# Kernel tuning notes

Hardware: AMD Instinct MI355X
Metric: run time of the kernel (lower is better)

Reference implementation:

```python
import jax, jax.numpy as jnp
import numpy as np

X_DIM = 512
Y_DIM = 512
HID = 300
N = 2048


def setup_inputs() -> dict:
    key = jax.random.key(0)
    ks = jax.random.split(key, 8)
    scale = 0.05
    return {
        "pos_local": jax.random.normal(ks[0], (N, X_DIM), jnp.float32),
        "pos_global": jax.random.normal(ks[1], (N, Y_DIM), jnp.float32),
        "neg_local": jax.random.normal(ks[2], (N, X_DIM), jnp.float32),
        "neg_global": jax.random.normal(ks[3], (N, Y_DIM), jnp.float32),
        "W1": jax.random.normal(ks[4], (X_DIM + Y_DIM, HID), jnp.float32) * scale,
        "b1": jnp.zeros((HID,), jnp.float32),
        "W2": jax.random.normal(ks[5], (HID, 1), jnp.float32) * scale,
        "b2": jnp.zeros((1,), jnp.float32),
        "batch_size": 256,
    }


def reference(pos_local, pos_global, neg_local, neg_global, W1, b1, W2, b2, batch_size):
    # Split first-layer weight into local/global halves so we never materialize
    # the concatenated pair tensor: F(cat(l, g)) uses l @ W1l + g @ W1g.
    W1l, W1g = W1[:X_DIM], W1[X_DIM:]
    w2, bias2 = W2[:, 0], b2[0]

    # Positive branch: plain batched MLP, chunking does not change the math.
    h0 = jax.nn.relu(pos_local @ W1l + pos_global @ W1g + b1)  # [N, HID]
    t0 = jax.nn.softplus(h0 @ w2 + bias2).mean()

    # Negative branch: per chunk of size B, pair (local_j, global_i),
    # score[i, j] = F(local_j, global_i); logsumexp over j, mean over i.
    nc = neg_local.shape[0] // batch_size
    nl = neg_local.reshape(nc, batch_size, X_DIM)
    ng = neg_global.reshape(nc, batch_size, Y_DIM)

    def chunk_term(carry, lg):
        l, g = lg                                   # [B, x], [B, y]
        lp = l @ W1l                                # [B, HID]
        gp = g @ W1g                                # [B, HID]
        h = jax.nn.relu(gp[:, None, :] + lp[None, :, :] + b1)  # [B, B, HID]
        s = jax.nn.softplus(h @ w2 + bias2)         # [B, B]
        val = jax.scipy.special.logsumexp(s, axis=1).mean()
        return carry + val, None

    total, _ = jax.lax.scan(chunk_term, jnp.float32(0.0), (nl, ng))
    t1 = total / nc

    lower_bound = t0 - t1
    return -lower_bound
```

## Files before the change

kernel.cpp:

```cpp
#include <hip/hip_runtime.h>
#include <math.h>

#define NR   2048
#define XD   512
#define HID  300
#define BS   256
#define NPAD 320
#define KTOT 1024
#define GSTR 304
#define HSTR 304
#define KP   320
#define NNEG 256

typedef __attribute__((ext_vector_type(8))) short bf16x8;
typedef __attribute__((ext_vector_type(4))) float f32x4;

__device__ __forceinline__ float softplus_f(float x) {
    return fmaxf(x, 0.f) + log1pf(__expf(-fabsf(x)));
}
__device__ __forceinline__ unsigned short f2bf(float f) {
    unsigned int u = __float_as_uint(f);
    u += 0x7FFFu + ((u >> 16) & 1u);
    return (unsigned short)(u >> 16);
}
__device__ __forceinline__ float bf2f(unsigned short h) {
    return __uint_as_float((unsigned int)h << 16);
}
__device__ __forceinline__ void unpk(unsigned int u, float& lo, float& hi) {
    lo = __uint_as_float(u << 16);
    hi = __uint_as_float(u & 0xFFFF0000u);
}

__global__ __launch_bounds__(256) void convert(
    const float* __restrict__ pl, const float* __restrict__ pg,
    const float* __restrict__ nl, const float* __restrict__ ng,
    const float* __restrict__ W1,
    unsigned short* __restrict__ Aneg, unsigned short* __restrict__ Apos,
    unsigned short* __restrict__ Wt, unsigned int* __restrict__ counter)
{
    const int b = blockIdx.x, tid = threadIdx.x;
    if (b == 0 && tid == 0) *counter = 0u;
    if (b < 4096) {
        const int m = (b < 2048) ? b : b - 2048;
        const float* lo = (b < 2048) ? nl : pl;
        const float* hi = (b < 2048) ? ng : pg;
        unsigned short* dst = (b < 2048) ? Aneg : Apos;
        const int kq = tid * 4;
        const float4 v = (kq < XD) ? *(const float4*)(lo + m * XD + kq)
                                   : *(const float4*)(hi + m * XD + kq - XD);
        ushort4 o;
        o.x = f2bf(v.x); o.y = f2bf(v.y); o.z = f2bf(v.z); o.w = f2bf(v.w);
        *(ushort4*)(dst + m * KTOT + kq) = o;
    } else {
        __shared__ unsigned short ts[16][72];
        const int t = b - 4096;
        const int nt = t % 20, kt = t / 20;
        const int n = nt * 16 + (tid & 15);
        const int kl = tid >> 4;
        #pragma unroll
        for (int j = 0; j < 4; ++j) {
            const int k = kt * 64 + kl * 4 + j;
            ts[tid & 15][kl * 4 + j] = f2bf((n < HID) ? W1[k * HID + n] : 0.f);
        }
        __syncthreads();
        const int nw = tid >> 4, kw = (tid & 15) * 4;
        ushort4 o;
        o.x = ts[nw][kw]; o.y = ts[nw][kw + 1]; o.z = ts[nw][kw + 2]; o.w = ts[nw][kw + 3];
        *(ushort4*)(Wt + (nt * 16 + nw) * KTOT + kt * 64 + kw) = o;
    }
}

__global__ __launch_bounds__(64) void mfma_gemm(
    const unsigned short* __restrict__ Aneg, const unsigned short* __restrict__ Apos,
    const unsigned short* __restrict__ Wt, const float* __restrict__ b1,
    unsigned short* __restrict__ LP4h, unsigned short* __restrict__ GPBh,
    float* __restrict__ P0a, float* __restrict__ P0b)
{
    const int bid = blockIdx.x;
    const int job = bid / 160, t = bid % 160;
    const int m0 = (t & 31) * 64, n0 = (t >> 5) * 64;
    const int lane = threadIdx.x;
    const int r = lane & 15, g = lane >> 4;

    const unsigned short* A = (job >= 2) ? Apos : Aneg;
    const int kbeg = (job & 1) ? XD : 0;

    const unsigned short* ap[4];
    const unsigned short* bp[4];
    #pragma unroll
    for (int mi = 0; mi < 4; ++mi)
        ap[mi] = A + (m0 + 16 * mi + r) * KTOT + kbeg + 8 * g;
    #pragma unroll
    for (int ni = 0; ni < 4; ++ni)
        bp[ni] = Wt + (n0 + 16 * ni + r) * KTOT + kbeg + 8 * g;

    f32x4 acc[4][4] = {};

    #pragma unroll 4
    for (int k = 0; k < XD; k += 32) {
        bf16x8 a[4], w[4];
        #pragma unroll
        for (int mi = 0; mi < 4; ++mi) a[mi] = *(const bf16x8*)(ap[mi] + k);
        #pragma unroll
        for (int ni = 0; ni < 4; ++ni) w[ni] = *(const bf16x8*)(bp[ni] + k);
        #pragma unroll
        for (int mi = 0; mi < 4; ++mi)
            #pragma unroll
            for (int ni = 0; ni < 4; ++ni)
                acc[mi][ni] = __builtin_amdgcn_mfma_f32_16x16x32_bf16(
                    a[mi], w[ni], acc[mi][ni], 0, 0, 0);
    }

    #pragma unroll
    for (int mi = 0; mi < 4; ++mi) {
        #pragma unroll
        for (int ni = 0; ni < 4; ++ni) {
            const int n = n0 + ni * 16 + r;
            const int mb = m0 + mi * 16 + 4 * g;
            const f32x4 v = acc[mi][ni];
            if (job == 0) {
                unsigned short* base = LP4h + ((size_t)(n >> 3) * NR + mb) * 8 + (n & 7);
                base[0]  = f2bf(v[0]); base[8]  = f2bf(v[1]);
                base[16] = f2bf(v[2]); base[24] = f2bf(v[3]);
            } else if (n < HID) {
                if (job == 1) {
                    const float bias = b1[n];
                    #pragma unroll
                    for (int j = 0; j < 4; ++j)
                        GPBh[(size_t)(mb + j) * HSTR + n] = f2bf(v[j] + bias);
                } else {
                    float* out = (job == 2) ? P0a : P0b;
                    #pragma unroll
                    for (int j = 0; j < 4; ++j)
                        out[(size_t)(mb + j) * GSTR + n] = v[j];
                }
            }
        }
    }
}

__global__ __launch_bounds__(512, 2) void negpos(
    const unsigned short* __restrict__ LP4h, const unsigned short* __restrict__ GPBh,
    const float* __restrict__ P0a, const float* __restrict__ P0b,
    const float* __restrict__ b1, const float* __restrict__ W2,
    const float* __restrict__ b2,
    float* __restrict__ negE, float* __restrict__ posP,
    unsigned int* __restrict__ counter, float* __restrict__ out)
{
    __shared__ __align__(16) float w2s[KP];
    __shared__ __align__(16) float gbs[8][KP];
    __shared__ __align__(16) float pacc[8][BS][8];
    __shared__ float sC[8];
    __shared__ float red[4][8];
    __shared__ float redp[8];
    __shared__ int sh_last;
    const int tid = threadIdx.x, bid = blockIdx.x;
    const int kh = tid >> 6, lh = tid & 63;
    const float b2v = b2[0];
    const int chunk = bid >> 5, g0 = (bid & 31) * 8;
    const size_t cb = (size_t)chunk * BS;

    const unsigned short* gpb = GPBh + (cb + g0) * HSTR;
    if (tid < KP) {
        const bool v = tid < HID;
        w2s[tid] = v ? 0.5f * W2[tid] : 0.f;
        #pragma unroll
        for (int g = 0; g < 8; ++g)
            gbs[g][tid] = v ? bf2f(gpb[g * HSTR + tid]) : 0.f;
    }
    __syncthreads();

    {
        float c = 0.f;
        #pragma unroll
        for (int h = 0; h < 2; ++h) {
            const int k4 = lh + 64 * h;
            if (k4 < 80) {
                const float4 g4 = *(const float4*)&gbs[kh][k4 * 4];
                const float4 w4 = *(const float4*)&w2s[k4 * 4];
                c += g4.x * w4.x + g4.y * w4.y + g4.z * w4.z + g4.w * w4.w;
            }
        }
        #pragma unroll
        for (int o = 32; o > 0; o >>= 1) c += __shfl_xor(c, o);
        if (lh == 0) sC[kh] = c;
    }

    float acc[8][4];
    float q[4] = {0.f, 0.f, 0.f, 0.f};
    #pragma unroll
    for (int gt = 0; gt < 8; ++gt)
        #pragma unroll
        for (int j = 0; j < 4; ++j) acc[gt][j] = 0.f;

    #pragma unroll
    for (int i = 0; i < 5; ++i) {
        const int k8 = 5 * kh + i;
        uint4 u0 = *(const uint4*)(LP4h + ((size_t)k8 * NR + cb + lh)       * 8);
        uint4 u1 = *(const uint4*)(LP4h + ((size_t)k8 * NR + cb + lh + 64)  * 8);
        uint4 u2 = *(const uint4*)(LP4h + ((size_t)k8 * NR + cb + lh + 128) * 8);
        uint4 u3 = *(const uint4*)(LP4h + ((size_t)k8 * NR + cb + lh + 192) * 8);
        const float4 wa = *(const float4*)&w2s[k8 * 8];
        const float4 wb = *(const float4*)&w2s[k8 * 8 + 4];
        float fv[4][8];
        unpk(u0.x, fv[0][0], fv[0][1]); unpk(u0.y, fv[0][2], fv[0][3]);
        unpk(u0.z, fv[0][4], fv[0][5]); unpk(u0.w, fv[0][6], fv[0][7]);
        unpk(u1.x, fv[1][0], fv[1][1]); unpk(u1.y, fv[1][2], fv[1][3]);
        unpk(u1.z, fv[1][4], fv[1][5]); unpk(u1.w, fv[1][6], fv[1][7]);
        unpk(u2.x, fv[2][0], fv[2][1]); unpk(u2.y, fv[2][2], fv[2][3]);
        unpk(u2.z, fv[2][4], fv[2][5]); unpk(u2.w, fv[2][6], fv[2][7]);
        unpk(u3.x, fv[3][0], fv[3][1]); unpk(u3.y, fv[3][2], fv[3][3]);
        unpk(u3.z, fv[3][4], fv[3][5]); unpk(u3.w, fv[3][6], fv[3][7]);
        #pragma unroll
        for (int j = 0; j < 4; ++j) {
            q[j] = fmaf(wa.x, fv[j][0], q[j]); q[j] = fmaf(wa.y, fv[j][1], q[j]);
            q[j] = fmaf(wa.z, fv[j][2], q[j]); q[j] = fmaf(wa.w, fv[j][3], q[j]);
            q[j] = fmaf(wb.x, fv[j][4], q[j]); q[j] = fmaf(wb.y, fv[j][5], q[j]);
            q[j] = fmaf(wb.z, fv[j][6], q[j]); q[j] = fmaf(wb.w, fv[j][7], q[j]);
        }
        #pragma unroll
        for (int gt = 0; gt < 8; ++gt) {
            const float4 ga = *(const float4*)&gbs[gt][k8 * 8];
            const float4 gb = *(const float4*)&gbs[gt][k8 * 8 + 4];
            #pragma unroll
            for (int j = 0; j < 4; ++j) {
                acc[gt][j] = fmaf(fabsf(ga.x + fv[j][0]), wa.x, acc[gt][j]);
                acc[gt][j] = fmaf(fabsf(ga.y + fv[j][1]), wa.y, acc[gt][j]);
                acc[gt][j] = fmaf(fabsf(ga.z + fv[j][2]), wa.z, acc[gt][j]);
                acc[gt][j] = fmaf(fabsf(ga.w + fv[j][3]), wa.w, acc[gt][j]);
                acc[gt][j] = fmaf(fabsf(gb.x + fv[j][4]), wb.x, acc[gt][j]);
                acc[gt][j] = fmaf(fabsf(gb.y + fv[j][5]), wb.y, acc[gt][j]);
                acc[gt][j] = fmaf(fabsf(gb.z + fv[j][6]), wb.z, acc[gt][j]);
                acc[gt][j] = fmaf(fabsf(gb.w + fv[j][7]), wb.w, acc[gt][j]);
            }
        }
    }

    #pragma unroll
    for (int j = 0; j < 4; ++j) {
        *(float4*)&pacc[kh][lh + 64 * j][0] =
            make_float4(acc[0][j] + q[j], acc[1][j] + q[j],
                        acc[2][j] + q[j], acc[3][j] + q[j]);
        *(float4*)&pacc[kh][lh + 64 * j][4] =
            make_float4(acc[4][j] + q[j], acc[5][j] + q[j],
                        acc[6][j] + q[j], acc[7][j] + q[j]);
    }
    __syncthreads();

    if (tid < 256) {
        float s[8];
        #pragma unroll
        for (int gt = 0; gt < 8; ++gt) s[gt] = sC[gt];
        #pragma unroll
        for (int k = 0; k < 8; ++k) {
            const float4 p0 = *(const float4*)&pacc[k][tid][0];
            const float4 p1 = *(const float4*)&pacc[k][tid][4];
            s[0] += p0.x; s[1] += p0.y; s[2] += p0.z; s[3] += p0.w;
            s[4] += p1.x; s[5] += p1.y; s[6] += p1.z; s[7] += p1.w;
        }
        const int wid = tid >> 6;
        #pragma unroll
        for (int gt = 0; gt < 8; ++gt) {
            float v = __expf(softplus_f(s[gt] + b2v));
            #pragma unroll
            for (int o = 32; o > 0; o >>= 1) v += __shfl_xor(v, o);
            if ((tid & 63) == 0) red[wid][gt] = v;
        }
    }
    __syncthreads();
    if (tid == 0) {
        #pragma unroll
        for (int gt = 0; gt < 8; ++gt)
            negE[bid * 8 + gt] = red[0][gt] + red[1][gt] + red[2][gt] + red[3][gt];
    }

    {
        const int row = bid * 8 + kh;
        const float4* ra = (const float4*)(P0a + (size_t)row * GSTR);
        const float4* rb = (const float4*)(P0b + (size_t)row * GSTR);
        float d = 0.f;
        #pragma unroll
        for (int h = 0; h < 2; ++h) {
            const int k4 = lh + 64 * h;
            if (k4 < 75) {
                const float4 aa = ra[k4], bb4 = rb[k4];
                const float4 bb = *(const float4*)(b1 + k4 * 4);
                const float4 wv = *(const float4*)(W2 + k4 * 4);
                d += fmaxf(aa.x + bb4.x + bb.x, 0.f) * wv.x
                   + fmaxf(aa.y + bb4.y + bb.y, 0.f) * wv.y
                   + fmaxf(aa.z + bb4.z + bb.z, 0.f) * wv.z
                   + fmaxf(aa.w + bb4.w + bb.w, 0.f) * wv.w;
            }
        }
        #pragma unroll
        for (int o = 32; o > 0; o >>= 1) d += __shfl_xor(d, o);
        if (lh == 0) redp[kh] = softplus_f(d + b2v);
    }
    __syncthreads();

    if (tid == 0) {
        posP[bid] = redp[0] + redp[1] + redp[2] + redp[3]
                  + redp[4] + redp[5] + redp[6] + redp[7];
        __threadfence();
        const unsigned t = atomicAdd(counter, 1u);
        sh_last = (t == NNEG - 1) ? 1 : 0;
    }
    __syncthreads();
    if (sh_last) {
        __threadfence();
        const volatile float* ne = (const volatile float*)negE;
        const volatile float* pp = (const volatile float*)posP;
        float v = 0.f;
        for (int i = tid; i < 2048; i += 512)
            v += __logf(ne[i]);
        if (tid < NNEG) v -= pp[tid];
        #pragma unroll
        for (int o = 32; o > 0; o >>= 1) v += __shfl_xor(v, o);
        if (lh == 0) redp[kh] = v;
        __syncthreads();
        if (tid == 0)
            out[0] = (redp[0] + redp[1] + redp[2] + redp[3]
                    + redp[4] + redp[5] + redp[6] + redp[7]) * (1.f / 2048.f);
    }
}

extern "C" void kernel_launch(void* const* d_in, const int* in_sizes, int n_in,
                              void* d_out, int out_size, void* d_ws, size_t ws_size,
                              hipStream_t stream)
{
    const float* pl = (const float*)d_in[0];
    const float* pg = (const float*)d_in[1];
    const float* nl = (const float*)d_in[2];
    const float* ng = (const float*)d_in[3];
    const float* W1 = (const float*)d_in[4];
    const float* b1 = (const float*)d_in[5];
    const float* W2 = (const float*)d_in[6];
    const float* b2 = (const float*)d_in[7];

    char* ws = (char*)d_ws;
    unsigned short* Aneg = (unsigned short*)(ws);
    unsigned short* Apos = (unsigned short*)(ws + (4u << 20));
    unsigned short* Wt   = (unsigned short*)(ws + (8u << 20));
    unsigned short* LP4h = (unsigned short*)(ws + (9u << 20));
    unsigned short* GPBh = (unsigned short*)(ws + (11u << 20));
    float* P0a  = (float*)(ws + (13u << 20));
    float* P0b  = (float*)(ws + (16u << 20));
    float* negE = (float*)(ws + (19u << 20));
    float* posP = negE + 2048;
    unsigned int* counter = (unsigned int*)(ws + (19u << 20) + 65536);
    float* out  = (float*)d_out;

    hipLaunchKernelGGL(convert, dim3(4096 + 320), dim3(256), 0, stream,
                       pl, pg, nl, ng, W1, Aneg, Apos, Wt, counter);
    hipLaunchKernelGGL(mfma_gemm, dim3(640), dim3(64), 0, stream,
                       Aneg, Apos, Wt, b1, LP4h, GPBh, P0a, P0b);
    hipLaunchKernelGGL(negpos, dim3(NNEG), dim3(512), 0, stream,
                       LP4h, GPBh, P0a, P0b, b1, W2, b2, negE, posP, counter, out);
}
```

Measured before the change: 58.88 us.

## Double-buffer local projections into LDS via async global_load_lds prefetch

Replaces the per-thread direct global loads of the bf16 local-projection tiles with a double-buffered LDS pipeline. Each stage is filled with global_load_lds while the previous stage is being computed, and the k-slices are reassigned so each iteration covers 8 consecutive k8 groups across the warps. The aim is to hide global memory latency behind the abs-FMA inner loop. It adds 64KB of LDS, which can lower blocks per CU, and a barrier on every iteration.

```diff
diff --git a/kernel.cpp b/kernel.cpp
--- a/kernel.cpp
+++ b/kernel.cpp
@@ -29,6 +29,11 @@
 __device__ __forceinline__ void unpk(unsigned int u, float& lo, float& hi) {
     lo = __uint_as_float(u << 16);
     hi = __uint_as_float(u & 0xFFFF0000u);
+}
+__device__ __forceinline__ void gload_lds16(const void* g, void* l) {
+    __builtin_amdgcn_global_load_lds(
+        (const __attribute__((address_space(1))) void*)g,
+        (__attribute__((address_space(3))) void*)l, 16, 0, 0);
 }
 
 __global__ __launch_bounds__(256) void convert(
@@ -147,6 +152,7 @@
     float* __restrict__ negE, float* __restrict__ posP,
     unsigned int* __restrict__ counter, float* __restrict__ out)
 {
+    __shared__ __align__(16) unsigned short lps[2][8][BS][8];
     __shared__ __align__(16) float w2s[KP];
     __shared__ __align__(16) float gbs[8][KP];
     __shared__ __align__(16) float pacc[8][BS][8];
@@ -168,6 +174,14 @@
         for (int g = 0; g < 8; ++g)
             gbs[g][tid] = v ? bf2f(gpb[g * HSTR + tid]) : 0.f;
     }
+
+    #pragma unroll
+    for (int i = 0; i < 4; ++i) {
+        const int c = i * 512 + tid;
+        const int k8l = c >> 8, l = c & 255;
+        gload_lds16(LP4h + ((size_t)k8l * NR + cb + l) * 8,
+                    &lps[0][k8l][l][0]);
+    }
     __syncthreads();
 
     {
@@ -194,14 +208,23 @@
         for (int j = 0; j < 4; ++j) acc[gt][j] = 0.f;
 
     #pragma unroll
-    for (int i = 0; i < 5; ++i) {
-        const int k8 = 5 * kh + i;
-        uint4 u0 = *(const uint4*)(LP4h + ((size_t)k8 * NR + cb + lh)       * 8);
-        uint4 u1 = *(const uint4*)(LP4h + ((size_t)k8 * NR + cb + lh + 64)  * 8);
-        uint4 u2 = *(const uint4*)(LP4h + ((size_t)k8 * NR + cb + lh + 128) * 8);
-        uint4 u3 = *(const uint4*)(LP4h + ((size_t)k8 * NR + cb + lh + 192) * 8);
-        const float4 wa = *(const float4*)&w2s[k8 * 8];
-        const float4 wb = *(const float4*)&w2s[k8 * 8 + 4];
+    for (int p = 0; p < 5; ++p) {
+        if (p < 4) {
+            #pragma unroll
+            for (int i = 0; i < 4; ++i) {
+                const int c = i * 512 + tid;
+                const int k8l = c >> 8, l = c & 255;
+                gload_lds16(LP4h + ((size_t)((p + 1) * 8 + k8l) * NR + cb + l) * 8,
+                            &lps[(p + 1) & 1][k8l][l][0]);
+            }
+        }
+        const int k8g = p * 8 + kh;
+        const uint4 u0 = *(const uint4*)&lps[p & 1][kh][lh][0];
+        const uint4 u1 = *(const uint4*)&lps[p & 1][kh][lh + 64][0];
+        const uint4 u2 = *(const uint4*)&lps[p & 1][kh][lh + 128][0];
+        const uint4 u3 = *(const uint4*)&lps[p & 1][kh][lh + 192][0];
+        const float4 wa = *(const float4*)&w2s[k8g * 8];
+        const float4 wb = *(const float4*)&w2s[k8g * 8 + 4];
         float fv[4][8];
         unpk(u0.x, fv[0][0], fv[0][1]); unpk(u0.y, fv[0][2], fv[0][3]);
         unpk(u0.z, fv[0][4], fv[0][5]); unpk(u0.w, fv[0][6], fv[0][7]);
@@ -220,8 +243,8 @@
         }
         #pragma unroll
         for (int gt = 0; gt < 8; ++gt) {
-            const float4 ga = *(const float4*)&gbs[gt][k8 * 8];
-            const float4 gb = *(const float4*)&gbs[gt][k8 * 8 + 4];
+            const float4 ga = *(const float4*)&gbs[gt][k8g * 8];
+            const float4 gb = *(const float4*)&gbs[gt][k8g * 8 + 4];
             #pragma unroll
             for (int j = 0; j < 4; ++j) {
                 acc[gt][j] = fmaf(fabsf(ga.x + fv[j][0]), wa.x, acc[gt][j]);
@@ -234,6 +257,7 @@
                 acc[gt][j] = fmaf(fabsf(gb.w + fv[j][7]), wb.w, acc[gt][j]);
             }
         }
+        __syncthreads();
     }
 
     #pragma unroll
```

Measured after the change: 64.44 us. 1.09x slower.
